# Optimization experiments

Measured on AMD Instinct MI355X. Metric: run time of the kernel, lower is better.

Reference implementation:

```python
import jax, jax.numpy as jnp
import numpy as np

N = 50000      # nodes
E = 800000     # edges
D_IN = 128
D_H = 128
D_OUT = 64


def _glorot(key, fan_in, fan_out):
    s = float(np.sqrt(6.0 / (fan_in + fan_out)))
    return jax.random.uniform(key, (fan_in, fan_out), jnp.float32, -s, s)


def setup_inputs() -> dict:
    key = jax.random.key(0)
    ks = jax.random.split(key, 8)
    x = jax.random.normal(ks[0], (N, D_IN), jnp.float32)
    edge_index = jax.random.randint(ks[1], (2, E), 0, N, dtype=jnp.int32)
    return {
        "x": x,
        "edge_index": edge_index,
        "W0": _glorot(ks[2], D_IN, D_H), "b0": jnp.zeros((D_H,), jnp.float32),
        "W1": _glorot(ks[3], D_H, D_H),  "b1": jnp.zeros((D_H,), jnp.float32),
        "W2": _glorot(ks[4], D_H, D_H),  "b2": jnp.zeros((D_H,), jnp.float32),
        "W_out": _glorot(ks[5], D_H, D_OUT), "b_out": jnp.zeros((D_OUT,), jnp.float32),
    }


def reference(x, edge_index, W0, b0, W1, b1, W2, b2, W_out, b_out):
    src = edge_index[0]
    dst = edge_index[1]
    # GCN normalization with self-loops: deg = in-degree(dst) + 1
    deg = jax.ops.segment_sum(jnp.ones((E,), x.dtype), dst, num_segments=N) + 1.0
    dinv = jax.lax.rsqrt(deg)                       # [N]
    edge_coef = (dinv[src] * dinv[dst])[:, None]    # [E,1]
    self_coef = (dinv * dinv)[:, None]              # [N,1]

    def gcn_conv(h, W, b):
        h = h @ W                                            # [N,F]
        agg = jax.ops.segment_sum(h[src] * edge_coef, dst, num_segments=N)
        agg = agg + h * self_coef                            # self-loop term
        return agg + b

    h = x
    for W, b in ((W0, b0), (W1, b1), (W2, b2)):
        h_in = h
        h = jax.nn.relu(gcn_conv(h, W, b))  # eval mode: dropout is identity
        if h.shape == h_in.shape:
            h = h + h_in
    return h @ W_out + b_out
```

## Files before the change

kernel.cpp:

```cpp
#include <hip/hip_runtime.h>

#define N_NODES 50000
#define N_EDGES 800000

static inline int cdiv(int a, int b) { return (a + b - 1) / b; }

typedef __attribute__((ext_vector_type(8))) short s8vec;
typedef __attribute__((ext_vector_type(4))) float f32x4;

__device__ inline ushort f2b(float f) {
    uint u = __float_as_uint(f);
    uint r = (u + 0x7fffu + ((u >> 16) & 1u)) >> 16;
    return (ushort)r;
}
__device__ inline float b2f_lo(uint v) { return __uint_as_float(v << 16); }
__device__ inline float b2f_hi(uint v) { return __uint_as_float(v & 0xffff0000u); }


__global__ __launch_bounds__(256) void k_zero_int(int* p, int n) {
    int i = blockIdx.x * 256 + threadIdx.x;
    if (i < n) p[i] = 0;
}

__global__ __launch_bounds__(256) void k_count(const int* __restrict__ dst, int* cnt, int e) {
    int i = blockIdx.x * 256 + threadIdx.x;
    if (i < e) atomicAdd(&cnt[dst[i]], 1);
}

__global__ __launch_bounds__(512) void k_block_sum(const int* __restrict__ cnt, int* bsum, int n) {
    __shared__ int sh[512];
    int i = blockIdx.x * 512 + threadIdx.x;
    sh[threadIdx.x] = (i < n) ? cnt[i] : 0;
    __syncthreads();
    for (int off = 256; off > 0; off >>= 1) {
        if (threadIdx.x < off) sh[threadIdx.x] += sh[threadIdx.x + off];
        __syncthreads();
    }
    if (threadIdx.x == 0) bsum[blockIdx.x] = sh[0];
}

__global__ __launch_bounds__(128) void k_scan_bsum(const int* __restrict__ bsum, int* boff,
                                                   int nb, int* rowptr, int n, int e) {
    __shared__ int sh[128];
    int t = threadIdx.x;
    int v = (t < nb) ? bsum[t] : 0;
    sh[t] = v;
    __syncthreads();
    for (int off = 1; off < 128; off <<= 1) {
        int add = (t >= off) ? sh[t - off] : 0;
        __syncthreads();
        sh[t] += add;
        __syncthreads();
    }
    if (t < nb) boff[t] = sh[t] - v;
    if (t == 0) rowptr[n] = e;
}

__global__ __launch_bounds__(512) void k_scan_block(const int* __restrict__ cnt,
                                                    const int* __restrict__ boff,
                                                    int* rowptr, int* cursor, float* dinv, int n) {
    __shared__ int sh[512];
    int t = threadIdx.x;
    int i = blockIdx.x * 512 + t;
    int v = (i < n) ? cnt[i] : 0;
    sh[t] = v;
    __syncthreads();
    for (int off = 1; off < 512; off <<= 1) {
        int add = (t >= off) ? sh[t - off] : 0;
        __syncthreads();
        sh[t] += add;
        __syncthreads();
    }
    if (i < n) {
        rowptr[i] = sh[t] - v + boff[blockIdx.x];
        cursor[i] = 0;
        dinv[i] = rsqrtf((float)v + 1.0f);
    }
}

__global__ __launch_bounds__(256) void k_fill(const int* __restrict__ src, const int* __restrict__ dst,
                                              const float* __restrict__ dinv,
                                              const int* __restrict__ rowptr, int* cursor,
                                              uint2* ed, int e) {
    int i = blockIdx.x * 256 + threadIdx.x;
    if (i >= e) return;
    int d = dst[i], s = src[i];
    int pos = rowptr[d] + atomicAdd(&cursor[d], 1);
    float c = dinv[s] * dinv[d];
    ed[pos] = make_uint2((uint)s, __float_as_uint(c));
}


__global__ __launch_bounds__(256) void k_wt_all(const float* __restrict__ W0, const float* __restrict__ W1,
                                                const float* __restrict__ W2, const float* __restrict__ Wo,
                                                ushort* Wt0, ushort* Wt1, ushort* Wt2, ushort* Wto) {
    int i = blockIdx.x * 256 + threadIdx.x;
    if (i < 16384) {
        int nn = i >> 7, k = i & 127;
        Wt0[i] = f2b(W0[k * 128 + nn]);
    } else if (i < 32768) {
        int j = i - 16384; int nn = j >> 7, k = j & 127;
        Wt1[j] = f2b(W1[k * 128 + nn]);
    } else if (i < 49152) {
        int j = i - 32768; int nn = j >> 7, k = j & 127;
        Wt2[j] = f2b(W2[k * 128 + nn]);
    } else if (i < 57344) {
        int j = i - 49152; int nn = j >> 7, k = j & 127;
        Wto[j] = f2b(Wo[k * 64 + nn]);
    }
}


template <int NCOL, bool IN_F32, bool OUT_F32>
__global__ __launch_bounds__(256) void k_mm(const void* __restrict__ Av,
                                            const ushort* __restrict__ Wt,
                                            const float* __restrict__ bias,
                                            void* __restrict__ Cv, int n) {
    constexpr int NT = NCOL / 16;
    int wave = threadIdx.x >> 6;
    int lane = threadIdx.x & 63;
    int quad = lane >> 4;
    int lm = lane & 15;
    int row0 = blockIdx.x * 128 + wave * 32;

    int rA0 = row0 + lm;      if (rA0 > n - 1) rA0 = n - 1;
    int rA1 = row0 + 16 + lm; if (rA1 > n - 1) rA1 = n - 1;

    f32x4 acc[2][NT];
#pragma unroll
    for (int r = 0; r < 2; r++)
#pragma unroll
        for (int t = 0; t < NT; t++) acc[r][t] = (f32x4){0.f, 0.f, 0.f, 0.f};

    for (int kc = 0; kc < 128; kc += 32) {
        s8vec af[2];
        if (IN_F32) {
            const float* A = (const float*)Av;
#pragma unroll
            for (int r = 0; r < 2; r++) {
                const float* p = A + (size_t)(r ? rA1 : rA0) * 128 + quad * 8 + kc;
                float4 a = *(const float4*)p, b = *(const float4*)(p + 4);
                s8vec v;
                v[0] = (short)f2b(a.x); v[1] = (short)f2b(a.y);
                v[2] = (short)f2b(a.z); v[3] = (short)f2b(a.w);
                v[4] = (short)f2b(b.x); v[5] = (short)f2b(b.y);
                v[6] = (short)f2b(b.z); v[7] = (short)f2b(b.w);
                af[r] = v;
            }
        } else {
            const ushort* A = (const ushort*)Av;
            af[0] = *(const s8vec*)(A + (size_t)rA0 * 128 + quad * 8 + kc);
            af[1] = *(const s8vec*)(A + (size_t)rA1 * 128 + quad * 8 + kc);
        }
#pragma unroll
        for (int t = 0; t < NT; t++) {
            s8vec bf = *(const s8vec*)(Wt + (size_t)(t * 16 + lm) * 128 + kc + quad * 8);
            acc[0][t] = __builtin_amdgcn_mfma_f32_16x16x32_bf16(af[0], bf, acc[0][t], 0, 0, 0);
            acc[1][t] = __builtin_amdgcn_mfma_f32_16x16x32_bf16(af[1], bf, acc[1][t], 0, 0, 0);
        }
    }

#pragma unroll
    for (int r = 0; r < 2; r++) {
#pragma unroll
        for (int t = 0; t < NT; t++) {
            int col = t * 16 + lm;
            float bv = OUT_F32 ? bias[col] : 0.f;
#pragma unroll
            for (int i = 0; i < 4; i++) {
                int rr = row0 + r * 16 + quad * 4 + i;
                if (rr < n) {
                    if (OUT_F32)
                        ((float*)Cv)[(size_t)rr * NCOL + col] = acc[r][t][i] + bv;
                    else
                        ((ushort*)Cv)[(size_t)rr * 128 + col] = f2b(acc[r][t][i]);
                }
            }
        }
    }
}


template <bool RES_F32>
__global__ __launch_bounds__(256) void k_gatherb(const uint* __restrict__ T,
                                                 const int* __restrict__ rowptr,
                                                 const uint2* __restrict__ ed,
                                                 const float* __restrict__ dinv,
                                                 const float* __restrict__ bias,
                                                 const void* __restrict__ resv,
                                                 uint* __restrict__ out, int n) {
    int node = blockIdx.x * 4 + (threadIdx.x >> 6);
    if (node >= n) return;
    int lane = threadIdx.x & 63;

    int beg = rowptr[node], end = rowptr[node + 1];
    float ax = 0.f, ay = 0.f;

    for (int base = beg; base < end; base += 64) {
        int m = end - base; if (m > 64) m = 64;
        uint2 em = make_uint2(0u, 0u);
        if (base + lane < end) em = ed[base + lane];
        int j = 0;
        for (; j + 4 <= m; j += 4) {
            int s0 = __shfl((int)em.x, j);
            int s1 = __shfl((int)em.x, j + 1);
            int s2 = __shfl((int)em.x, j + 2);
            int s3 = __shfl((int)em.x, j + 3);
            float c0 = __int_as_float(__shfl((int)em.y, j));
            float c1 = __int_as_float(__shfl((int)em.y, j + 1));
            float c2 = __int_as_float(__shfl((int)em.y, j + 2));
            float c3 = __int_as_float(__shfl((int)em.y, j + 3));
            uint v0 = T[(size_t)s0 * 64 + lane];
            uint v1 = T[(size_t)s1 * 64 + lane];
            uint v2 = T[(size_t)s2 * 64 + lane];
            uint v3 = T[(size_t)s3 * 64 + lane];
            ax += b2f_lo(v0) * c0 + b2f_lo(v1) * c1 + b2f_lo(v2) * c2 + b2f_lo(v3) * c3;
            ay += b2f_hi(v0) * c0 + b2f_hi(v1) * c1 + b2f_hi(v2) * c2 + b2f_hi(v3) * c3;
        }
        for (; j < m; j++) {
            int s = __shfl((int)em.x, j);
            float c = __int_as_float(__shfl((int)em.y, j));
            uint v = T[(size_t)s * 64 + lane];
            ax += b2f_lo(v) * c;
            ay += b2f_hi(v) * c;
        }
    }

    float di = dinv[node];
    float sc = di * di;
    uint vs = T[(size_t)node * 64 + lane];
    float2 b = ((const float2*)bias)[lane];
    ax += b2f_lo(vs) * sc + b.x;
    ay += b2f_hi(vs) * sc + b.y;

    float rx, ry;
    if (RES_F32) {
        float2 rv = ((const float2*)resv)[(size_t)node * 64 + lane];
        rx = rv.x; ry = rv.y;
    } else {
        uint rv = ((const uint*)resv)[(size_t)node * 64 + lane];
        rx = b2f_lo(rv); ry = b2f_hi(rv);
    }
    float ox = fmaxf(ax, 0.f) + rx;
    float oy = fmaxf(ay, 0.f) + ry;
    out[(size_t)node * 64 + lane] = (uint)f2b(ox) | ((uint)f2b(oy) << 16);
}


extern "C" void kernel_launch(void* const* d_in, const int* in_sizes, int n_in,
                              void* d_out, int out_size, void* d_ws, size_t ws_size,
                              hipStream_t stream) {
    const float* x  = (const float*)d_in[0];
    const int* eidx = (const int*)d_in[1];
    const float* W0 = (const float*)d_in[2];
    const float* b0 = (const float*)d_in[3];
    const float* W1 = (const float*)d_in[4];
    const float* b1 = (const float*)d_in[5];
    const float* W2 = (const float*)d_in[6];
    const float* b2 = (const float*)d_in[7];
    const float* Wo = (const float*)d_in[8];
    const float* bo = (const float*)d_in[9];
    float* out = (float*)d_out;

    const int N = N_NODES, E = N_EDGES;
    const int* srcI = eidx;
    const int* dstI = eidx + E;
    const int NB512 = cdiv(N, 512);

    char* ws = (char*)d_ws;
    auto alloc = [&](size_t bytes) { char* p = ws; ws += (bytes + 255) / 256 * 256; return p; };
    int*    cnt    = (int*)alloc((size_t)N * 4);
    int*    cursor = (int*)alloc((size_t)N * 4);
    int*    rowptr = (int*)alloc((size_t)(N + 1) * 4);
    int*    bsum   = (int*)alloc((size_t)NB512 * 4);
    int*    boff   = (int*)alloc((size_t)NB512 * 4);
    float*  dinv   = (float*)alloc((size_t)N * 4);
    uint2*  ed     = (uint2*)alloc((size_t)E * 8);
    ushort* tmpb   = (ushort*)alloc((size_t)N * 128 * 2);
    ushort* hAb    = (ushort*)alloc((size_t)N * 128 * 2);
    ushort* hBb    = (ushort*)alloc((size_t)N * 128 * 2);
    ushort* Wt0    = (ushort*)alloc(128 * 128 * 2);
    ushort* Wt1    = (ushort*)alloc(128 * 128 * 2);
    ushort* Wt2    = (ushort*)alloc(128 * 128 * 2);
    ushort* Wto    = (ushort*)alloc(64 * 128 * 2);

    dim3 b256(256), b512(512);

    k_zero_int<<<cdiv(N, 256), b256, 0, stream>>>(cnt, N);
    k_count<<<cdiv(E, 256), b256, 0, stream>>>(dstI, cnt, E);
    k_block_sum<<<NB512, b512, 0, stream>>>(cnt, bsum, N);
    k_scan_bsum<<<1, 128, 0, stream>>>(bsum, boff, NB512, rowptr, N, E);
    k_scan_block<<<NB512, b512, 0, stream>>>(cnt, boff, rowptr, cursor, dinv, N);
    k_fill<<<cdiv(E, 256), b256, 0, stream>>>(srcI, dstI, dinv, rowptr, cursor, ed, E);
    k_wt_all<<<cdiv(57344, 256), b256, 0, stream>>>(W0, W1, W2, Wo, Wt0, Wt1, Wt2, Wto);

    const int mmGrid = cdiv(N, 128);
    const int gGrid  = cdiv(N, 4);

    k_mm<128, true, false><<<mmGrid, b256, 0, stream>>>(x, Wt0, nullptr, tmpb, N);
    k_gatherb<true><<<gGrid, b256, 0, stream>>>((const uint*)tmpb, rowptr, ed, dinv, b0, x, (uint*)hAb, N);

    k_mm<128, false, false><<<mmGrid, b256, 0, stream>>>(hAb, Wt1, nullptr, tmpb, N);
    k_gatherb<false><<<gGrid, b256, 0, stream>>>((const uint*)tmpb, rowptr, ed, dinv, b1, hAb, (uint*)hBb, N);

    k_mm<128, false, false><<<mmGrid, b256, 0, stream>>>(hBb, Wt2, nullptr, tmpb, N);
    k_gatherb<false><<<gGrid, b256, 0, stream>>>((const uint*)tmpb, rowptr, ed, dinv, b2, hBb, (uint*)hAb, N);

    k_mm<64, false, true><<<mmGrid, b256, 0, stream>>>(hAb, Wto, bo, out, N);
}
```

Baseline: 338.1 us.

## Use 16-lane-per-node uint4 gather and merge setup kernels into fewer launches

The aggregation kernel now gives each node 16 lanes that load 16-byte uint4 rows, so one wave handles four nodes instead of one, with shuffles offset per 16-lane group. Zeroing the count buffer is folded into the weight-transpose kernel, and the CSR fill kernel is merged into the first matmul launch as extra blocks. The intent is more memory-level parallelism per wave for the short adjacency lists (average degree about 16) and fewer kernel launches. In exchange each lane holds more registers, and nodes of different degree in one wave can diverge.

```diff
diff --git a/kernel.cpp b/kernel.cpp
--- a/kernel.cpp
+++ b/kernel.cpp
@@ -16,85 +16,25 @@
 __device__ inline float b2f_lo(uint v) { return __uint_as_float(v << 16); }
 __device__ inline float b2f_hi(uint v) { return __uint_as_float(v & 0xffff0000u); }
 
-
-__global__ __launch_bounds__(256) void k_zero_int(int* p, int n) {
-    int i = blockIdx.x * 256 + threadIdx.x;
-    if (i < n) p[i] = 0;
-}
-
-__global__ __launch_bounds__(256) void k_count(const int* __restrict__ dst, int* cnt, int e) {
-    int i = blockIdx.x * 256 + threadIdx.x;
-    if (i < e) atomicAdd(&cnt[dst[i]], 1);
-}
-
-__global__ __launch_bounds__(512) void k_block_sum(const int* __restrict__ cnt, int* bsum, int n) {
-    __shared__ int sh[512];
-    int i = blockIdx.x * 512 + threadIdx.x;
-    sh[threadIdx.x] = (i < n) ? cnt[i] : 0;
-    __syncthreads();
-    for (int off = 256; off > 0; off >>= 1) {
-        if (threadIdx.x < off) sh[threadIdx.x] += sh[threadIdx.x + off];
-        __syncthreads();
-    }
-    if (threadIdx.x == 0) bsum[blockIdx.x] = sh[0];
-}
-
-__global__ __launch_bounds__(128) void k_scan_bsum(const int* __restrict__ bsum, int* boff,
-                                                   int nb, int* rowptr, int n, int e) {
-    __shared__ int sh[128];
-    int t = threadIdx.x;
-    int v = (t < nb) ? bsum[t] : 0;
-    sh[t] = v;
-    __syncthreads();
-    for (int off = 1; off < 128; off <<= 1) {
-        int add = (t >= off) ? sh[t - off] : 0;
-        __syncthreads();
-        sh[t] += add;
-        __syncthreads();
-    }
-    if (t < nb) boff[t] = sh[t] - v;
-    if (t == 0) rowptr[n] = e;
-}
-
-__global__ __launch_bounds__(512) void k_scan_block(const int* __restrict__ cnt,
-                                                    const int* __restrict__ boff,
-                                                    int* rowptr, int* cursor, float* dinv, int n) {
-    __shared__ int sh[512];
-    int t = threadIdx.x;
-    int i = blockIdx.x * 512 + t;
-    int v = (i < n) ? cnt[i] : 0;
-    sh[t] = v;
-    __syncthreads();
-    for (int off = 1; off < 512; off <<= 1) {
-        int add = (t >= off) ? sh[t - off] : 0;
-        __syncthreads();
-        sh[t] += add;
-        __syncthreads();
-    }
-    if (i < n) {
-        rowptr[i] = sh[t] - v + boff[blockIdx.x];
-        cursor[i] = 0;
-        dinv[i] = rsqrtf((float)v + 1.0f);
-    }
-}
-
-__global__ __launch_bounds__(256) void k_fill(const int* __restrict__ src, const int* __restrict__ dst,
-                                              const float* __restrict__ dinv,
-                                              const int* __restrict__ rowptr, int* cursor,
-                                              uint2* ed, int e) {
-    int i = blockIdx.x * 256 + threadIdx.x;
-    if (i >= e) return;
-    int d = dst[i], s = src[i];
-    int pos = rowptr[d] + atomicAdd(&cursor[d], 1);
-    float c = dinv[s] * dinv[d];
-    ed[pos] = make_uint2((uint)s, __float_as_uint(c));
-}
-
-
-__global__ __launch_bounds__(256) void k_wt_all(const float* __restrict__ W0, const float* __restrict__ W1,
-                                                const float* __restrict__ W2, const float* __restrict__ Wo,
-                                                ushort* Wt0, ushort* Wt1, ushort* Wt2, ushort* Wto) {
-    int i = blockIdx.x * 256 + threadIdx.x;
+__device__ inline void acc8(float* acc, uint4 v, float c) {
+    acc[0] += b2f_lo(v.x) * c; acc[1] += b2f_hi(v.x) * c;
+    acc[2] += b2f_lo(v.y) * c; acc[3] += b2f_hi(v.y) * c;
+    acc[4] += b2f_lo(v.z) * c; acc[5] += b2f_hi(v.z) * c;
+    acc[6] += b2f_lo(v.w) * c; acc[7] += b2f_hi(v.w) * c;
+}
+
+
+__global__ __launch_bounds__(256) void k_prep(int* cnt,
+                                              const float* __restrict__ W0, const float* __restrict__ W1,
+                                              const float* __restrict__ W2, const float* __restrict__ Wo,
+                                              ushort* Wt0, ushort* Wt1, ushort* Wt2, ushort* Wto) {
+    int b = blockIdx.x;
+    if (b < 196) {
+        int i = b * 256 + threadIdx.x;
+        if (i < N_NODES) cnt[i] = 0;
+        return;
+    }
+    int i = (b - 196) * 256 + threadIdx.x;
     if (i < 16384) {
         int nn = i >> 7, k = i & 127;
         Wt0[i] = f2b(W0[k * 128 + nn]);
@@ -110,18 +50,74 @@
     }
 }
 
+__global__ __launch_bounds__(256) void k_count(const int* __restrict__ dst, int* cnt, int e) {
+    int i = blockIdx.x * 256 + threadIdx.x;
+    if (i < e) atomicAdd(&cnt[dst[i]], 1);
+}
+
+
+__global__ __launch_bounds__(512) void k_block_sum(const int* __restrict__ cnt, int* bsum, int n) {
+    __shared__ int sh[512];
+    int i = blockIdx.x * 512 + threadIdx.x;
+    sh[threadIdx.x] = (i < n) ? cnt[i] : 0;
+    __syncthreads();
+    for (int off = 256; off > 0; off >>= 1) {
+        if (threadIdx.x < off) sh[threadIdx.x] += sh[threadIdx.x + off];
+        __syncthreads();
+    }
+    if (threadIdx.x == 0) bsum[blockIdx.x] = sh[0];
+}
+
+__global__ __launch_bounds__(128) void k_scan_bsum(const int* __restrict__ bsum, int* boff,
+                                                   int nb, int* rowptr, int n, int e) {
+    __shared__ int sh[128];
+    int t = threadIdx.x;
+    int v = (t < nb) ? bsum[t] : 0;
+    sh[t] = v;
+    __syncthreads();
+    for (int off = 1; off < 128; off <<= 1) {
+        int add = (t >= off) ? sh[t - off] : 0;
+        __syncthreads();
+        sh[t] += add;
+        __syncthreads();
+    }
+    if (t < nb) boff[t] = sh[t] - v;
+    if (t == 0) rowptr[n] = e;
+}
+
+__global__ __launch_bounds__(512) void k_scan_block(const int* __restrict__ cnt,
+                                                    const int* __restrict__ boff,
+                                                    int* rowptr, int* cursor, float* dinv, int n) {
+    __shared__ int sh[512];
+    int t = threadIdx.x;
+    int i = blockIdx.x * 512 + t;
+    int v = (i < n) ? cnt[i] : 0;
+    sh[t] = v;
+    __syncthreads();
+    for (int off = 1; off < 512; off <<= 1) {
+        int add = (t >= off) ? sh[t - off] : 0;
+        __syncthreads();
+        sh[t] += add;
+        __syncthreads();
+    }
+    if (i < n) {
+        rowptr[i] = sh[t] - v + boff[blockIdx.x];
+        cursor[i] = 0;
+        dinv[i] = rsqrtf((float)v + 1.0f);
+    }
+}
+
 
 template <int NCOL, bool IN_F32, bool OUT_F32>
-__global__ __launch_bounds__(256) void k_mm(const void* __restrict__ Av,
-                                            const ushort* __restrict__ Wt,
-                                            const float* __restrict__ bias,
-                                            void* __restrict__ Cv, int n) {
+__device__ inline void mm_body(const void* __restrict__ Av, const ushort* __restrict__ Wt,
+                               const float* __restrict__ bias, void* __restrict__ Cv,
+                               int n, int bid) {
     constexpr int NT = NCOL / 16;
     int wave = threadIdx.x >> 6;
     int lane = threadIdx.x & 63;
     int quad = lane >> 4;
     int lm = lane & 15;
-    int row0 = blockIdx.x * 128 + wave * 32;
+    int row0 = bid * 128 + wave * 32;
 
     int rA0 = row0 + lm;      if (rA0 > n - 1) rA0 = n - 1;
     int rA1 = row0 + 16 + lm; if (rA1 > n - 1) rA1 = n - 1;
@@ -180,70 +176,112 @@
     }
 }
 
+template <int NCOL, bool IN_F32, bool OUT_F32>
+__global__ __launch_bounds__(256) void k_mm(const void* __restrict__ Av,
+                                            const ushort* __restrict__ Wt,
+                                            const float* __restrict__ bias,
+                                            void* __restrict__ Cv, int n) {
+    mm_body<NCOL, IN_F32, OUT_F32>(Av, Wt, bias, Cv, n, blockIdx.x);
+}
+
+__global__ __launch_bounds__(256) void k_mm0_fill(const void* __restrict__ Av,
+                                                  const ushort* __restrict__ Wt,
+                                                  void* __restrict__ Cv, int n, int mmblocks,
+                                                  const int* __restrict__ src, const int* __restrict__ dst,
+                                                  const float* __restrict__ dinv,
+                                                  const int* __restrict__ rowptr, int* cursor,
+                                                  uint2* ed, int e) {
+    if ((int)blockIdx.x >= mmblocks) {
+        int i = ((int)blockIdx.x - mmblocks) * 256 + threadIdx.x;
+        if (i < e) {
+            int d = dst[i], s = src[i];
+            int pos = rowptr[d] + atomicAdd(&cursor[d], 1);
+            float c = dinv[s] * dinv[d];
+            ed[pos] = make_uint2((uint)s, __float_as_uint(c));
+        }
+        return;
+    }
+    mm_body<128, true, false>(Av, Wt, nullptr, Cv, n, blockIdx.x);
+}
+
 
 template <bool RES_F32>
-__global__ __launch_bounds__(256) void k_gatherb(const uint* __restrict__ T,
+__global__ __launch_bounds__(256) void k_gatherb(const uint4* __restrict__ T4,
                                                  const int* __restrict__ rowptr,
                                                  const uint2* __restrict__ ed,
                                                  const float* __restrict__ dinv,
                                                  const float* __restrict__ bias,
                                                  const void* __restrict__ resv,
-                                                 uint* __restrict__ out, int n) {
-    int node = blockIdx.x * 4 + (threadIdx.x >> 6);
+                                                 uint4* __restrict__ out4, int n) {
+    int node = blockIdx.x * 16 + (threadIdx.x >> 4);
     if (node >= n) return;
-    int lane = threadIdx.x & 63;
-
+    int ql = threadIdx.x & 15;
+    int qb = threadIdx.x & 48;
+
+    float acc[8] = {0.f, 0.f, 0.f, 0.f, 0.f, 0.f, 0.f, 0.f};
     int beg = rowptr[node], end = rowptr[node + 1];
-    float ax = 0.f, ay = 0.f;
-
-    for (int base = beg; base < end; base += 64) {
-        int m = end - base; if (m > 64) m = 64;
+
+    for (int base = beg; base < end; base += 16) {
+        int m = end - base; if (m > 16) m = 16;
         uint2 em = make_uint2(0u, 0u);
-        if (base + lane < end) em = ed[base + lane];
+        if (base + ql < end) em = ed[base + ql];
         int j = 0;
         for (; j + 4 <= m; j += 4) {
-            int s0 = __shfl((int)em.x, j);
-            int s1 = __shfl((int)em.x, j + 1);
-            int s2 = __shfl((int)em.x, j + 2);
-            int s3 = __shfl((int)em.x, j + 3);
-            float c0 = __int_as_float(__shfl((int)em.y, j));
-            float c1 = __int_as_float(__shfl((int)em.y, j + 1));
-            float c2 = __int_as_float(__shfl((int)em.y, j + 2));
-            float c3 = __int_as_float(__shfl((int)em.y, j + 3));
-            uint v0 = T[(size_t)s0 * 64 + lane];
-            uint v1 = T[(size_t)s1 * 64 + lane];
-            uint v2 = T[(size_t)s2 * 64 + lane];
-            uint v3 = T[(size_t)s3 * 64 + lane];
-            ax += b2f_lo(v0) * c0 + b2f_lo(v1) * c1 + b2f_lo(v2) * c2 + b2f_lo(v3) * c3;
-            ay += b2f_hi(v0) * c0 + b2f_hi(v1) * c1 + b2f_hi(v2) * c2 + b2f_hi(v3) * c3;
+            int s0 = __shfl((int)em.x, qb + j);
+            int s1 = __shfl((int)em.x, qb + j + 1);
+            int s2 = __shfl((int)em.x, qb + j + 2);
+            int s3 = __shfl((int)em.x, qb + j + 3);
+            float c0 = __uint_as_float((uint)__shfl((int)em.y, qb + j));
+            float c1 = __uint_as_float((uint)__shfl((int)em.y, qb + j + 1));
+            float c2 = __uint_as_float((uint)__shfl((int)em.y, qb + j + 2));
+            float c3 = __uint_as_float((uint)__shfl((int)em.y, qb + j + 3));
+            uint4 v0 = T4[(size_t)s0 * 16 + ql];
+            uint4 v1 = T4[(size_t)s1 * 16 + ql];
+            uint4 v2 = T4[(size_t)s2 * 16 + ql];
+            uint4 v3 = T4[(size_t)s3 * 16 + ql];
+            acc8(acc, v0, c0); acc8(acc, v1, c1);
+            acc8(acc, v2, c2); acc8(acc, v3, c3);
         }
         for (; j < m; j++) {
-            int s = __shfl((int)em.x, j);
-            float c = __int_as_float(__shfl((int)em.y, j));
-            uint v = T[(size_t)s * 64 + lane];
-            ax += b2f_lo(v) * c;
-            ay += b2f_hi(v) * c;
+            int s = __shfl((int)em.x, qb + j);
+            float c = __uint_as_float((uint)__shfl((int)em.y, qb + j));
+            uint4 v = T4[(size_t)s * 16 + ql];
+            acc8(acc, v, c);
         }
     }
 
     float di = dinv[node];
     float sc = di * di;
-    uint vs = T[(size_t)node * 64 + lane];
-    float2 b = ((const float2*)bias)[lane];
-    ax += b2f_lo(vs) * sc + b.x;
-    ay += b2f_hi(vs) * sc + b.y;
-
-    float rx, ry;
+    uint4 vs = T4[(size_t)node * 16 + ql];
+    float self[8] = {b2f_lo(vs.x), b2f_hi(vs.x), b2f_lo(vs.y), b2f_hi(vs.y),
+                     b2f_lo(vs.z), b2f_hi(vs.z), b2f_lo(vs.w), b2f_hi(vs.w)};
+    float4 bv0 = ((const float4*)bias)[ql * 2];
+    float4 bv1 = ((const float4*)bias)[ql * 2 + 1];
+    float bb[8] = {bv0.x, bv0.y, bv0.z, bv0.w, bv1.x, bv1.y, bv1.z, bv1.w};
+
+    float r[8];
     if (RES_F32) {
-        float2 rv = ((const float2*)resv)[(size_t)node * 64 + lane];
-        rx = rv.x; ry = rv.y;
+        float4 r0 = ((const float4*)resv)[(size_t)node * 32 + ql * 2];
+        float4 r1 = ((const float4*)resv)[(size_t)node * 32 + ql * 2 + 1];
+        r[0] = r0.x; r[1] = r0.y; r[2] = r0.z; r[3] = r0.w;
+        r[4] = r1.x; r[5] = r1.y; r[6] = r1.z; r[7] = r1.w;
     } else {
-        uint rv = ((const uint*)resv)[(size_t)node * 64 + lane];
-        rx = b2f_lo(rv); ry = b2f_hi(rv);
-    }
-    float ox = fmaxf(ax, 0.f) + rx;
-    float oy = fmaxf(ay, 0.f) + ry;
-    out[(size_t)node * 64 + lane] = (uint)f2b(ox) | ((uint)f2b(oy) << 16);
+        uint4 rv = ((const uint4*)resv)[(size_t)node * 16 + ql];
+        r[0] = b2f_lo(rv.x); r[1] = b2f_hi(rv.x); r[2] = b2f_lo(rv.y); r[3] = b2f_hi(rv.y);
+        r[4] = b2f_lo(rv.z); r[5] = b2f_hi(rv.z); r[6] = b2f_lo(rv.w); r[7] = b2f_hi(rv.w);
+    }
+
+    float o[8];
+#pragma unroll
+    for (int i = 0; i < 8; i++)
+        o[i] = fmaxf(acc[i] + self[i] * sc + bb[i], 0.f) + r[i];
+
+    uint4 ov;
+    ov.x = (uint)f2b(o[0]) | ((uint)f2b(o[1]) << 16);
+    ov.y = (uint)f2b(o[2]) | ((uint)f2b(o[3]) << 16);
+    ov.z = (uint)f2b(o[4]) | ((uint)f2b(o[5]) << 16);
+    ov.w = (uint)f2b(o[6]) | ((uint)f2b(o[7]) << 16);
+    out4[(size_t)node * 16 + ql] = ov;
 }
 
 
@@ -286,25 +324,25 @@
 
     dim3 b256(256), b512(512);
 
-    k_zero_int<<<cdiv(N, 256), b256, 0, stream>>>(cnt, N);
+    const int mmGrid = cdiv(N, 128);
+    const int fillGrid = cdiv(E, 256);
+    const int gGrid = cdiv(N, 16);
+
+    k_prep<<<196 + 224, b256, 0, stream>>>(cnt, W0, W1, W2, Wo, Wt0, Wt1, Wt2, Wto);
     k_count<<<cdiv(E, 256), b256, 0, stream>>>(dstI, cnt, E);
     k_block_sum<<<NB512, b512, 0, stream>>>(cnt, bsum, N);
     k_scan_bsum<<<1, 128, 0, stream>>>(bsum, boff, NB512, rowptr, N, E);
     k_scan_block<<<NB512, b512, 0, stream>>>(cnt, boff, rowptr, cursor, dinv, N);
-    k_fill<<<cdiv(E, 256), b256, 0, stream>>>(srcI, dstI, dinv, rowptr, cursor, ed, E);
-    k_wt_all<<<cdiv(57344, 256), b256, 0, stream>>>(W0, W1, W2, Wo, Wt0, Wt1, Wt2, Wto);
-
-    const int mmGrid = cdiv(N, 128);
-    const int gGrid  = cdiv(N, 4);
-
-    k_mm<128, true, false><<<mmGrid, b256, 0, stream>>>(x, Wt0, nullptr, tmpb, N);
-    k_gatherb<true><<<gGrid, b256, 0, stream>>>((const uint*)tmpb, rowptr, ed, dinv, b0, x, (uint*)hAb, N);
+
+    k_mm0_fill<<<mmGrid + fillGrid, b256, 0, stream>>>(x, Wt0, tmpb, N, mmGrid,
+                                                       srcI, dstI, dinv, rowptr, cursor, ed, E);
+    k_gatherb<true><<<gGrid, b256, 0, stream>>>((const uint4*)tmpb, rowptr, ed, dinv, b0, x, (uint4*)hAb, N);
 
     k_mm<128, false, false><<<mmGrid, b256, 0, stream>>>(hAb, Wt1, nullptr, tmpb, N);
-    k_gatherb<false><<<gGrid, b256, 0, stream>>>((const uint*)tmpb, rowptr, ed, dinv, b1, hAb, (uint*)hBb, N);
+    k_gatherb<false><<<gGrid, b256, 0, stream>>>((const uint4*)tmpb, rowptr, ed, dinv, b1, hAb, (uint4*)hBb, N);
 
     k_mm<128, false, false><<<mmGrid, b256, 0, stream>>>(hBb, Wt2, nullptr, tmpb, N);
-    k_gatherb<false><<<gGrid, b256, 0, stream>>>((const uint*)tmpb, rowptr, ed, dinv, b2, hBb, (uint*)hAb, N);
+    k_gatherb<false><<<gGrid, b256, 0, stream>>>((const uint4*)tmpb, rowptr, ed, dinv, b2, hBb, (uint4*)hAb, N);
 
     k_mm<64, false, true><<<mmGrid, b256, 0, stream>>>(hAb, Wto, bo, out, N);
 }
```

Result: faster. 312.1 us (-7.7%).
